# Optimization experiments

Measured on AMD Instinct MI355X. Metric: run time of the kernel, lower is better.

Reference implementation:

```python
import jax, jax.numpy as jnp
import numpy as np

D = 256; N_GRU = 4; L = 3; RATIO = 0.8; B = 64; PAD = 0
VOCAB = 50000; N = 20000; E = 320000; T = 16


def setup_inputs() -> dict:
    key = jax.random.key(0)
    ks = jax.random.split(key, 10)
    s = 0.05
    return {
        "x_tokens": jax.random.randint(ks[0], (N, T), 0, VOCAB),
        "edge_index": jax.random.randint(ks[1], (2, E), 0, N),
        "batch": jnp.sort(jax.random.randint(ks[2], (N,), 0, B)),
        "embed": jax.random.normal(ks[3], (VOCAB, D)) * s,
        "ggc_W": jax.random.normal(ks[4], (L, N_GRU, D, D)) * s,
        "gru_Wih": jax.random.normal(ks[5], (L, 3 * D, D)) * s,
        "gru_Whh": jax.random.normal(ks[6], (L, 3 * D, D)) * s,
        "gru_bih": jnp.zeros((L, 3 * D)),
        "gru_bhh": jnp.zeros((L, 3 * D)),
        "topk_p": jax.random.normal(ks[7], (L, D)) * s,
        "gate_W": jax.random.normal(ks[8], (D, 1)) * s,
        "gate_b": jnp.zeros((1,)),
    }


def gru_cell(m, h, Wih, Whh, bih, bhh):
    gi = m @ Wih.T + bih
    gh = h @ Whh.T + bhh
    i_r, i_z, i_n = jnp.split(gi, 3, axis=-1)
    h_r, h_z, h_n = jnp.split(gh, 3, axis=-1)
    r = jax.nn.sigmoid(i_r + h_r)
    z = jax.nn.sigmoid(i_z + h_z)
    n = jnp.tanh(i_n + r * h_n)
    return (1.0 - z) * n + z * h


def gated_graph_conv(h, src, dst, emask, W, Wih, Whh, bih, bhh):
    # PyG GatedGraphConv: per step, transform then scatter-add source->target, then GRU update
    for l in range(N_GRU):
        msg = (h @ W[l])[src] * emask[:, None]            # [E, D]
        agg = jax.ops.segment_sum(msg, dst, num_segments=h.shape[0])
        h = gru_cell(agg, h, Wih, Whh, bih, bhh)
    return h


def topk_pool(x, p, nmask, batch, src, dst, emask):
    # PyG TopKPooling: score = tanh(x.p/||p||), keep top ceil(ratio*n) per graph, x *= score
    score = jnp.tanh((x @ p) / jnp.linalg.norm(p))
    skey = jnp.where(nmask, score, -1e9)
    order = jnp.lexsort((-skey, batch))                   # by graph asc, score desc
    counts = jax.ops.segment_sum(jnp.ones((N,), jnp.int32), batch, num_segments=B)
    starts = jnp.cumsum(counts) - counts
    rank = jnp.zeros((N,), jnp.int32).at[order].set(
        jnp.arange(N, dtype=jnp.int32) - starts[batch[order]])
    n_valid = jax.ops.segment_sum(nmask.astype(jnp.int32), batch, num_segments=B)
    k = jnp.ceil(RATIO * n_valid.astype(jnp.float32)).astype(jnp.int32)
    keep = nmask & (rank < k[batch])
    x_new = jnp.where(keep[:, None], x * score[:, None], 0.0)
    emask_new = emask * keep[src].astype(emask.dtype) * keep[dst].astype(emask.dtype)
    return x_new, keep, emask_new


def global_att(x, nmask, batch, gW, gb):
    # GlobalAttention: segment softmax of Linear(x,1), weighted sum per graph
    logit = jnp.where(nmask, (x @ gW)[:, 0] + gb[0], -1e9)
    mx = jax.ops.segment_max(logit, batch, num_segments=B)
    e = jnp.where(nmask, jnp.exp(logit - mx[batch]), 0.0)
    denom = jax.ops.segment_sum(e, batch, num_segments=B)
    gate = e / jnp.maximum(denom[batch], 1e-12)
    return jax.ops.segment_sum(gate[:, None] * x, batch, num_segments=B)


def reference(x_tokens, edge_index, batch, embed, ggc_W, gru_Wih, gru_Whh,
              gru_bih, gru_bhh, topk_p, gate_W, gate_b):
    # STEncoder: embed token ids, mean-pool non-pad tokens per node
    tok_mask = (x_tokens != PAD)
    emb = embed[x_tokens] * tok_mask[..., None]
    h = emb.sum(1) / jnp.maximum(tok_mask.sum(1, keepdims=True), 1).astype(emb.dtype)
    src, dst = edge_index[0], edge_index[1]
    nmask = jnp.ones((N,), bool)
    emask = jnp.ones((E,), h.dtype)
    out = jnp.zeros((B, D), h.dtype)
    for l in range(L):
        h = jax.nn.relu(gated_graph_conv(h, src, dst, emask, ggc_W[l],
                                         gru_Wih[l], gru_Whh[l], gru_bih[l], gru_bhh[l]))
        h, nmask, emask = topk_pool(h, topk_p[l], nmask, batch, src, dst, emask)
        out = out + global_att(h, nmask, batch, gate_W, gate_b)
    return out
```

## Files before the change

### kernel.cpp

```cpp
#include <hip/hip_runtime.h>
#include <hip/hip_bf16.h>

namespace {

constexpr int NN = 20000;
constexpr int TT = 16;
constexpr int DD = 256;
constexpr int EE = 320000;
constexpr int BB = 64;
constexpr int NLAY = 3;
constexpr int NGRUS = 4;
constexpr int D3 = 768;
constexpr int NRB = 157;
constexpr int NXCD = 8;

typedef __bf16 bf16x8 __attribute__((ext_vector_type(8)));
typedef float  f32x4  __attribute__((ext_vector_type(4)));

__device__ __forceinline__ float us2f(unsigned short u){
  union { unsigned int i; float f; } v; v.i = ((unsigned int)u) << 16; return v.f;
}
__device__ __forceinline__ unsigned short f2us(float f){
  union { float f; unsigned int i; } v; v.f = f;
  unsigned int r = v.i + 0x7fff + ((v.i >> 16) & 1);
  return (unsigned short)(r >> 16);
}

__device__ __forceinline__ void gload16(const unsigned short* g, unsigned short* l){
  __builtin_amdgcn_global_load_lds(
      (const __attribute__((address_space(1))) unsigned int*)g,
      (__attribute__((address_space(3))) unsigned int*)l, 16, 0, 0);
}

__global__ void k_init(int* __restrict__ deg, int* __restrict__ cursor,
                       int* __restrict__ nmask, float* __restrict__ out){
  int i = blockIdx.x*256 + threadIdx.x;
  if (i < NN){ deg[i] = 0; cursor[i] = 0; nmask[i] = 1; }
  if (i < BB*DD) out[i] = 0.f;
}

__global__ void k_embed(const int* __restrict__ xt, const float* __restrict__ emb,
                        unsigned short* __restrict__ h){
  int n = blockIdx.x; int d = threadIdx.x;
  __shared__ int toks[TT];
  if (threadIdx.x < TT) toks[threadIdx.x] = xt[n*TT + threadIdx.x];
  __syncthreads();
  float acc = 0.f; int cnt = 0;
  #pragma unroll
  for (int t = 0; t < TT; ++t){
    int tk = toks[t];
    if (tk != 0){ ++cnt; acc += emb[(size_t)tk*DD + d]; }
  }
  h[(size_t)n*DD + d] = f2us(acc / (float)(cnt > 0 ? cnt : 1));
}

__global__ __launch_bounds__(256) void k_wf(const float* __restrict__ W,
                                            const float* __restrict__ Wih,
                                            unsigned short* __restrict__ WFThi,
                                            unsigned short* __restrict__ WFTlo){
  int lg = blockIdx.z; int l = lg / NGRUS;
  const float* A  = W   + (size_t)lg*DD*DD;
  const float* Bm = Wih + (size_t)l*D3*DD;
  unsigned short* oh = WFThi + (size_t)lg*D3*DD;
  unsigned short* ol = WFTlo + (size_t)lg*D3*DD;
  int k0 = blockIdx.y*64, j0 = blockIdx.x*64;
  __shared__ float sA[16][68], sB[16][68];
  int tid = threadIdx.x, ty = tid/16, tx = tid%16;
  float acc[4][4] = {};
  int m = tid >> 2, dg = (tid & 3)*4;
  for (int d0 = 0; d0 < DD; d0 += 16){
    float4 ua = *reinterpret_cast<const float4*>(A  + (size_t)(k0+m)*DD + d0+dg);
    float4 ub = *reinterpret_cast<const float4*>(Bm + (size_t)(j0+m)*DD + d0+dg);
    __syncthreads();
    sA[dg+0][m]=ua.x; sA[dg+1][m]=ua.y; sA[dg+2][m]=ua.z; sA[dg+3][m]=ua.w;
    sB[dg+0][m]=ub.x; sB[dg+1][m]=ub.y; sB[dg+2][m]=ub.z; sB[dg+3][m]=ub.w;
    __syncthreads();
    #pragma unroll
    for (int dd = 0; dd < 16; ++dd){
      float a[4], b[4];
      #pragma unroll
      for (int i=0;i<4;++i) a[i] = sA[dd][ty*4+i];
      #pragma unroll
      for (int j=0;j<4;++j) b[j] = sB[dd][tx*4+j];
      #pragma unroll
      for (int i=0;i<4;++i)
        #pragma unroll
        for (int j=0;j<4;++j) acc[i][j] += a[i]*b[j];
    }
  }
  for (int i=0;i<4;++i){
    int k = k0 + ty*4 + i;
    for (int j=0;j<4;++j){
      int c = j0 + tx*4 + j;
      float v = acc[i][j];
      unsigned short hi = f2us(v);
      float rem = v - us2f(hi);
      oh[(size_t)c*DD + k] = hi;
      ol[(size_t)c*DD + k] = f2us(rem);
    }
  }
}

__global__ void k_whh_split(const float* __restrict__ Whh, unsigned short* __restrict__ hi,
                            unsigned short* __restrict__ lo){
  size_t i = (size_t)blockIdx.x*256 + threadIdx.x;
  if (i >= (size_t)NLAY*D3*DD) return;
  float w = Whh[i];
  unsigned short h = f2us(w);
  hi[i] = h; lo[i] = f2us(w - us2f(h));
}

__global__ void k_deg(const int* __restrict__ dst, int* __restrict__ deg){
  int e = blockIdx.x*256 + threadIdx.x; if (e < EE) atomicAdd(&deg[dst[e]], 1);
}
__global__ void k_scan(const int* __restrict__ deg, int* __restrict__ offs){
  __shared__ int part[1024];
  int t = threadIdx.x; const int CH = 20;
  int base = t*CH; int s = 0;
  for (int i = 0; i < CH; ++i){ int idx = base+i; if (idx < NN) s += deg[idx]; }
  part[t] = s; __syncthreads();
  for (int o = 1; o < 1024; o <<= 1){
    int v = part[t]; int add = (t >= o) ? part[t-o] : 0;
    __syncthreads(); part[t] = v + add; __syncthreads();
  }
  int run = (t > 0) ? part[t-1] : 0;
  for (int i = 0; i < CH; ++i){ int idx = base+i; if (idx < NN){ offs[idx] = run; run += deg[idx]; } }
  if (t == 1023) offs[NN] = run;
}
__global__ void k_fill_csr(const int* __restrict__ src, const int* __restrict__ dst,
                           const int* __restrict__ offs, int* __restrict__ cursor,
                           int* __restrict__ csr_src){
  int e = blockIdx.x*256 + threadIdx.x; if (e >= EE) return;
  int d = dst[e]; int pos = atomicAdd(&cursor[d], 1);
  csr_src[offs[d] + pos] = src[e];
}

__global__ void k_bounds(const int* __restrict__ batch, int* __restrict__ starts65){
  int n = blockIdx.x*256 + threadIdx.x;
  if (n >= NN) return;
  int b = batch[n];
  int p = (n == 0) ? -1 : batch[n-1];
  for (int bb = p+1; bb <= b; ++bb) starts65[bb] = n;
  if (n == NN-1){
    for (int bb = b+1; bb <= BB; ++bb) starts65[bb] = NN;
  }
}
__global__ void k_cnts(const int* __restrict__ starts65, int* __restrict__ counts){
  int b = threadIdx.x;
  if (b < BB) counts[b] = starts65[b+1] - starts65[b];
}

__global__ void k_agg(const unsigned short* __restrict__ h, const int* __restrict__ offs,
                      const int* __restrict__ csr_src, unsigned short* __restrict__ agg){
  int wid = threadIdx.x >> 6, lane = threadIdx.x & 63;
  int n = blockIdx.x*4 + wid;
  if (n >= NN) return;
  int s = offs[n], e = offs[n+1];
  float a0 = 0.f, a1 = 0.f, a2 = 0.f, a3 = 0.f;
  int slot = s;
  for (; slot + 2 <= e; slot += 2){
    int s0 = csr_src[slot], s1 = csr_src[slot+1];
    ushort4 v0 = *reinterpret_cast<const ushort4*>(h + (size_t)s0*DD + lane*4);
    ushort4 v1 = *reinterpret_cast<const ushort4*>(h + (size_t)s1*DD + lane*4);
    a0 += us2f(v0.x) + us2f(v1.x);
    a1 += us2f(v0.y) + us2f(v1.y);
    a2 += us2f(v0.z) + us2f(v1.z);
    a3 += us2f(v0.w) + us2f(v1.w);
  }
  if (slot < e){
    int s0 = csr_src[slot];
    ushort4 v0 = *reinterpret_cast<const ushort4*>(h + (size_t)s0*DD + lane*4);
    a0 += us2f(v0.x); a1 += us2f(v0.y); a2 += us2f(v0.z); a3 += us2f(v0.w);
  }
  ushort4 o;
  o.x = f2us(a0); o.y = f2us(a1); o.z = f2us(a2); o.w = f2us(a3);
  *reinterpret_cast<ushort4*>(agg + (size_t)n*DD + lane*4) = o;
}

__global__ __launch_bounds__(256) void k_gru(
    const unsigned short* __restrict__ Ag, const unsigned short* __restrict__ Ah,
    const unsigned short* __restrict__ WfH, const unsigned short* __restrict__ WfL,
    const unsigned short* __restrict__ WhH, const unsigned short* __restrict__ WhL,
    const float* __restrict__ bih, const float* __restrict__ bhh,
    const int* __restrict__ nmask, unsigned short* __restrict__ Hn, int do_relu){
  __shared__ unsigned short sB[2][2][96*64];
  int t = threadIdx.x;
  int wv = t >> 6, lane = t & 63;
  int lr = lane & 15, kg = lane >> 4;

  int w = blockIdx.x;
  int q = (w & 7)*NRB + (w >> 3);
  int r0 = (q >> 3) * 128;
  int g0 = q & 7;

  int sw   = ((lane & 7) ^ (lane >> 3)) * 8;
  int rloc = lane >> 3;

  auto stageBoth = [&](int buf, int a){
    const unsigned short* mH = (a & 4) ? WhH : WfH;
    const unsigned short* mL = (a & 4) ? WhL : WfL;
    int kin0 = (a & 3) * 64;
    #pragma unroll
    for (int i = 0; i < 3; ++i){
      int brow = (wv + i*4)*8;
      int gate = brow >> 5;
      size_t srow = (size_t)(gate*256 + g0*32 + (brow & 31) + rloc)*DD + kin0 + sw;
      gload16(mH + srow, &sB[buf][0][brow*64]);
      gload16(mL + srow, &sB[buf][1][brow*64]);
    }
  };

  f32x4 aR[2][2], aZ[2][2], aNi[2][2], aNh[2][2];
  #pragma unroll
  for (int rf = 0; rf < 2; ++rf)
    #pragma unroll
    for (int h2 = 0; h2 < 2; ++h2){
      aR[rf][h2] = (f32x4){0.f,0.f,0.f,0.f};  aZ[rf][h2] = (f32x4){0.f,0.f,0.f,0.f};
      aNi[rf][h2] = (f32x4){0.f,0.f,0.f,0.f}; aNh[rf][h2] = (f32x4){0.f,0.f,0.f,0.f};
    }

  size_t arow0 = (size_t)(r0 + wv*32 + lr) * DD;
  size_t arow1 = (size_t)(r0 + wv*32 + 16 + lr) * DD;

  bf16x8 aF0[2][2], aF1[2][2];
  #pragma unroll
  for (int kk2 = 0; kk2 < 2; ++kk2){
    aF0[0][kk2] = *reinterpret_cast<const bf16x8*>(Ag + arow0 + kk2*32 + kg*8);
    aF1[0][kk2] = *reinterpret_cast<const bf16x8*>(Ag + arow1 + kk2*32 + kg*8);
  }
  stageBoth(0, 0);

  #pragma unroll
  for (int a = 0; a < 8; ++a){
    int buf = a & 1;
    int par = a & 1;
    __syncthreads();
    if (a < 7){
      stageBoth(buf ^ 1, a + 1);
      const unsigned short* An = ((a+1) & 4) ? Ah : Ag;
      int kinn = ((a+1) & 3) * 64;
      #pragma unroll
      for (int kk2 = 0; kk2 < 2; ++kk2){
        aF0[par ^ 1][kk2] = *reinterpret_cast<const bf16x8*>(An + arow0 + kinn + kk2*32 + kg*8);
        aF1[par ^ 1][kk2] = *reinterpret_cast<const bf16x8*>(An + arow1 + kinn + kk2*32 + kg*8);
      }
    }
    int half = (a >> 2) & 1;
    __builtin_amdgcn_s_setprio(1);
    #pragma unroll
    for (int ph = 0; ph < 2; ++ph){
      #pragma unroll
      for (int kk2 = 0; kk2 < 2; ++kk2){
        int cs = ((kk2*4 + kg) ^ (lr & 7)) * 8;
        bf16x8 a0 = aF0[par][kk2];
        bf16x8 a1 = aF1[par][kk2];
        #pragma unroll
        for (int h2 = 0; h2 < 2; ++h2){
          bf16x8 bR = *reinterpret_cast<const bf16x8*>(&sB[buf][ph][(      h2*16 + lr)*64 + cs]);
          bf16x8 bZ = *reinterpret_cast<const bf16x8*>(&sB[buf][ph][(32  + h2*16 + lr)*64 + cs]);
          bf16x8 bN = *reinterpret_cast<const bf16x8*>(&sB[buf][ph][(64  + h2*16 + lr)*64 + cs]);
          aR[0][h2] = __builtin_amdgcn_mfma_f32_16x16x32_bf16(a0, bR, aR[0][h2], 0, 0, 0);
          aR[1][h2] = __builtin_amdgcn_mfma_f32_16x16x32_bf16(a1, bR, aR[1][h2], 0, 0, 0);
          aZ[0][h2] = __builtin_amdgcn_mfma_f32_16x16x32_bf16(a0, bZ, aZ[0][h2], 0, 0, 0);
          aZ[1][h2] = __builtin_amdgcn_mfma_f32_16x16x32_bf16(a1, bZ, aZ[1][h2], 0, 0, 0);
          if (half){
            aNh[0][h2] = __builtin_amdgcn_mfma_f32_16x16x32_bf16(a0, bN, aNh[0][h2], 0, 0, 0);
            aNh[1][h2] = __builtin_amdgcn_mfma_f32_16x16x32_bf16(a1, bN, aNh[1][h2], 0, 0, 0);
          } else {
            aNi[0][h2] = __builtin_amdgcn_mfma_f32_16x16x32_bf16(a0, bN, aNi[0][h2], 0, 0, 0);
            aNi[1][h2] = __builtin_amdgcn_mfma_f32_16x16x32_bf16(a1, bN, aNi[1][h2], 0, 0, 0);
          }
        }
      }
    }
    __builtin_amdgcn_s_setprio(0);
  }

  #pragma unroll
  for (int h2 = 0; h2 < 2; ++h2){
    int col = g0*32 + h2*16 + lr;
    float bRv = bih[col]       + bhh[col];
    float bZv = bih[256 + col] + bhh[256 + col];
    float bN1 = bih[512 + col];
    float bN2 = bhh[512 + col];
    #pragma unroll
    for (int rf = 0; rf < 2; ++rf){
      #pragma unroll
      for (int j = 0; j < 4; ++j){
        int row = r0 + wv*32 + rf*16 + kg*4 + j;
        if (row < NN){
          float r = 1.f/(1.f + expf(-(aR[rf][h2][j] + bRv)));
          float z = 1.f/(1.f + expf(-(aZ[rf][h2][j] + bZv)));
          float nv = tanhf(aNi[rf][h2][j] + bN1 + r*(aNh[rf][h2][j] + bN2));
          float ho = us2f(Ah[(size_t)row*DD + col]);
          float o = (1.f - z)*nv + z*ho;
          if (do_relu) o = fmaxf(o, 0.f);
          if (!nmask[row]) o = 0.f;
          Hn[(size_t)row*DD + col] = f2us(o);
        }
      }
    }
  }
}

__global__ void k_score(const unsigned short* __restrict__ h, const float* __restrict__ p,
                        float* __restrict__ score){
  int wid = threadIdx.x >> 6, lane = threadIdx.x & 63;
  int n = blockIdx.x*4 + wid; if (n >= NN) return;
  ushort4 hu = *reinterpret_cast<const ushort4*>(h + (size_t)n*DD + lane*4);
  float4 pv = *reinterpret_cast<const float4*>(p + lane*4);
  float dot = us2f(hu.x)*pv.x + us2f(hu.y)*pv.y + us2f(hu.z)*pv.z + us2f(hu.w)*pv.w;
  float pp = pv.x*pv.x + pv.y*pv.y + pv.z*pv.z + pv.w*pv.w;
  for (int o = 32; o; o >>= 1){ dot += __shfl_down(dot, o); pp += __shfl_down(pp, o); }
  if (lane == 0) score[n] = tanhf(dot / sqrtf(pp));
}

__global__ void k_topk(const float* __restrict__ score, const int* __restrict__ starts,
                       const int* __restrict__ counts, int* __restrict__ nmask){
  int b = blockIdx.x; int st = starts[b]; int cnt = min(counts[b], 1024);
  __shared__ float sc[1024]; __shared__ int ired[256];
  int t = threadIdx.x;
  int myvalid = 0;
  for (int i = t; i < cnt; i += 256){
    int node = st + i; int v = nmask[node];
    sc[i] = v ? score[node] : -1e30f;
    myvalid += v;
  }
  ired[t] = myvalid; __syncthreads();
  for (int o = 128; o; o >>= 1){ if (t < o) ired[t] += ired[t+o]; __syncthreads(); }
  int nv = ired[0];
  int k = (4*nv + 4)/5;
  __syncthreads();
  for (int i = t; i < cnt; i += 256){
    float si = sc[i]; int node = st + i; int keep = 0;
    if (si > -1e29f){
      int rank = 0;
      for (int j = 0; j < cnt; ++j){
        float sj = sc[j];
        rank += (sj > si) || (sj == si && j < i);
      }
      keep = (rank < k);
    }
    nmask[node] = keep;
  }
}

__global__ void k_scale(unsigned short* __restrict__ h, const float* __restrict__ score,
                        const int* __restrict__ nmask){
  int idx = blockIdx.x*256 + threadIdx.x;
  int n = idx >> 8;
  unsigned short v = nmask[n] ? f2us(us2f(h[idx])*score[n]) : (unsigned short)0;
  h[idx] = v;
}

__global__ void k_att(const unsigned short* __restrict__ h, const float* __restrict__ gW,
                      const float* __restrict__ gb, const int* __restrict__ starts,
                      const int* __restrict__ counts, const int* __restrict__ nmask,
                      float* __restrict__ outacc){
  int b = blockIdx.x; int st = starts[b]; int cnt = min(counts[b], 1024);
  __shared__ float lg[1024]; __shared__ float red[256];
  int t = threadIdx.x, wid = t >> 6, lane = t & 63;
  float gbv = gb[0];
  for (int i = wid; i < cnt; i += 4){
    int node = st + i;
    ushort4 hu = *reinterpret_cast<const ushort4*>(h + (size_t)node*DD + lane*4);
    float4 wv = *reinterpret_cast<const float4*>(gW + lane*4);
    float dot = us2f(hu.x)*wv.x + us2f(hu.y)*wv.y + us2f(hu.z)*wv.z + us2f(hu.w)*wv.w;
    for (int o = 32; o; o >>= 1) dot += __shfl_down(dot, o);
    if (lane == 0) lg[i] = nmask[node] ? dot + gbv : -1e30f;
  }
  __syncthreads();
  float mx = -1e30f;
  for (int i = t; i < cnt; i += 256) mx = fmaxf(mx, lg[i]);
  red[t] = mx; __syncthreads();
  for (int o = 128; o; o >>= 1){ if (t < o) red[t] = fmaxf(red[t], red[t+o]); __syncthreads(); }
  mx = red[0]; __syncthreads();
  float se = 0.f;
  for (int i = t; i < cnt; i += 256){
    float e = (lg[i] > -1e29f) ? expf(lg[i] - mx) : 0.f;
    lg[i] = e; se += e;
  }
  red[t] = se; __syncthreads();
  for (int o = 128; o; o >>= 1){ if (t < o) red[t] += red[t+o]; __syncthreads(); }
  float denom = fmaxf(red[0], 1e-12f);
  __syncthreads();
  float a0=0.f,a1=0.f,a2=0.f,a3=0.f;
  int i = 0;
  for (; i + 4 <= cnt; i += 4){
    a0 += lg[i+0]*us2f(h[(size_t)(st+i+0)*DD + t]);
    a1 += lg[i+1]*us2f(h[(size_t)(st+i+1)*DD + t]);
    a2 += lg[i+2]*us2f(h[(size_t)(st+i+2)*DD + t]);
    a3 += lg[i+3]*us2f(h[(size_t)(st+i+3)*DD + t]);
  }
  for (; i < cnt; ++i) a0 += lg[i]*us2f(h[(size_t)(st+i)*DD + t]);
  outacc[(size_t)b*DD + t] += (a0+a1+a2+a3)/denom;
}

}

extern "C" void kernel_launch(void* const* d_in, const int* in_sizes, int n_in,
                              void* d_out, int out_size, void* d_ws, size_t ws_size,
                              hipStream_t stream){
  const int*   x_tokens = (const int*)d_in[0];
  const int*   e_src    = (const int*)d_in[1];
  const int*   e_dst    = e_src + EE;
  const int*   batch    = (const int*)d_in[2];
  const float* embed    = (const float*)d_in[3];
  const float* ggcW     = (const float*)d_in[4];
  const float* gWih     = (const float*)d_in[5];
  const float* gWhh     = (const float*)d_in[6];
  const float* gbih     = (const float*)d_in[7];
  const float* gbhh     = (const float*)d_in[8];
  const float* topkp    = (const float*)d_in[9];
  const float* gateW    = (const float*)d_in[10];
  const float* gateb    = (const float*)d_in[11];
  (void)in_sizes; (void)n_in; (void)out_size;
  float* out = (float*)d_out;

  char* ws = (char*)d_ws;
  size_t off = 0;
  auto carve = [&](size_t bytes)->char*{
    char* p = ws + off;
    off += (bytes + 255) & ~(size_t)255;
    return p;
  };
  unsigned short* h0    = (unsigned short*)carve((size_t)NN*DD*2);
  unsigned short* h1    = (unsigned short*)carve((size_t)NN*DD*2);
  unsigned short* agg   = (unsigned short*)carve((size_t)NN*DD*2);
  unsigned short* WFThi = (unsigned short*)carve((size_t)NLAY*NGRUS*D3*DD*2);
  unsigned short* WFTlo = (unsigned short*)carve((size_t)NLAY*NGRUS*D3*DD*2);
  unsigned short* WhhHi = (unsigned short*)carve((size_t)NLAY*D3*DD*2);
  unsigned short* WhhLo = (unsigned short*)carve((size_t)NLAY*D3*DD*2);
  float* score   = (float*)carve((size_t)NN*4);
  int* nmask     = (int*)carve((size_t)NN*4);
  int* deg       = (int*)carve((size_t)NN*4);
  int* cursor    = (int*)carve((size_t)NN*4);
  int* offs      = (int*)carve((size_t)(NN+1)*4);
  int* csr_src   = (int*)carve((size_t)EE*4);
  int* counts    = (int*)carve((size_t)BB*4);
  int* starts    = (int*)carve((size_t)(BB+1)*4);
  if (off > ws_size) return;

  k_init<<<(NN+255)/256, 256, 0, stream>>>(deg, cursor, nmask, out);
  k_embed<<<NN, DD, 0, stream>>>(x_tokens, embed, h0);
  k_wf<<<dim3(D3/64, DD/64, NLAY*NGRUS), 256, 0, stream>>>(ggcW, gWih, WFThi, WFTlo);
  k_whh_split<<<(NLAY*D3*DD + 255)/256, 256, 0, stream>>>(gWhh, WhhHi, WhhLo);
  k_deg<<<(EE+255)/256, 256, 0, stream>>>(e_dst, deg);
  k_scan<<<1, 1024, 0, stream>>>(deg, offs);
  k_fill_csr<<<(EE+255)/256, 256, 0, stream>>>(e_src, e_dst, offs, cursor, csr_src);
  k_bounds<<<(NN+255)/256, 256, 0, stream>>>(batch, starts);
  k_cnts<<<1, 64, 0, stream>>>(starts, counts);

  unsigned short* hc = h0; unsigned short* hn = h1;
  for (int l = 0; l < NLAY; ++l){
    const unsigned short* WhHl = WhhHi + (size_t)l*D3*DD;
    const unsigned short* WhLl = WhhLo + (size_t)l*D3*DD;
    const float* bihl = gbih + (size_t)l*D3;
    const float* bhhl = gbhh + (size_t)l*D3;
    for (int g = 0; g < NGRUS; ++g){
      const unsigned short* WfHl = WFThi + (size_t)(l*NGRUS+g)*D3*DD;
      const unsigned short* WfLl = WFTlo + (size_t)(l*NGRUS+g)*D3*DD;
      k_agg<<<(NN+3)/4, 256, 0, stream>>>(hc, offs, csr_src, agg);
      k_gru<<<NRB*NXCD, 256, 0, stream>>>(agg, hc, WfHl, WfLl, WhHl, WhLl,
                                          bihl, bhhl, nmask, hn,
                                          (g == NGRUS-1) ? 1 : 0);
      unsigned short* tmp = hc; hc = hn; hn = tmp;
    }
    k_score<<<NN/4, 256, 0, stream>>>(hc, topkp + (size_t)l*DD, score);
    k_topk<<<BB, 256, 0, stream>>>(score, starts, counts, nmask);
    k_scale<<<NN, 256, 0, stream>>>(hc, score, nmask);
    k_att<<<BB, 256, 0, stream>>>(hc, gateW, gateb, starts, counts, nmask, out);
  }
}
```

Measured before the change: 1.374 ms.

## Double GRU row tile to 256 and batch CSR index loads in aggregation

The fused GRU GEMM kernel now gives each block 256 rows instead of 128. Each wave handles four 16-row fragments, so every staged weight tile in LDS is reused across twice as many rows, and the grid shrinks accordingly. The neighbour aggregation kernel now loads up to 64 CSR source indices per wave in one coalesced load, broadcasts them with shuffles, and unrolls the gather four deep. The larger tile raises accumulator and A-fragment register use, which may lower occupancy. A small padding buffer is added to the workspace to absorb the out-of-range row reads from the last tile.

```diff
diff --git a/kernel.cpp b/kernel.cpp
--- a/kernel.cpp
+++ b/kernel.cpp
@@ -11,7 +11,7 @@
 constexpr int NLAY = 3;
 constexpr int NGRUS = 4;
 constexpr int D3 = 768;
-constexpr int NRB = 157;
+constexpr int NRB2 = 79;
 constexpr int NXCD = 8;
 
 typedef __bf16 bf16x8 __attribute__((ext_vector_type(8)));
@@ -157,20 +157,27 @@
   if (n >= NN) return;
   int s = offs[n], e = offs[n+1];
   float a0 = 0.f, a1 = 0.f, a2 = 0.f, a3 = 0.f;
-  int slot = s;
-  for (; slot + 2 <= e; slot += 2){
-    int s0 = csr_src[slot], s1 = csr_src[slot+1];
-    ushort4 v0 = *reinterpret_cast<const ushort4*>(h + (size_t)s0*DD + lane*4);
-    ushort4 v1 = *reinterpret_cast<const ushort4*>(h + (size_t)s1*DD + lane*4);
-    a0 += us2f(v0.x) + us2f(v1.x);
-    a1 += us2f(v0.y) + us2f(v1.y);
-    a2 += us2f(v0.z) + us2f(v1.z);
-    a3 += us2f(v0.w) + us2f(v1.w);
-  }
-  if (slot < e){
-    int s0 = csr_src[slot];
-    ushort4 v0 = *reinterpret_cast<const ushort4*>(h + (size_t)s0*DD + lane*4);
-    a0 += us2f(v0.x); a1 += us2f(v0.y); a2 += us2f(v0.z); a3 += us2f(v0.w);
+  for (int base = s; base < e; base += 64){
+    int cnt = min(64, e - base);
+    int idx = (lane < cnt) ? csr_src[base + lane] : 0;
+    int i = 0;
+    for (; i + 4 <= cnt; i += 4){
+      int s0 = __shfl(idx, i+0), s1 = __shfl(idx, i+1);
+      int s2 = __shfl(idx, i+2), s3 = __shfl(idx, i+3);
+      ushort4 v0 = *reinterpret_cast<const ushort4*>(h + (size_t)s0*DD + lane*4);
+      ushort4 v1 = *reinterpret_cast<const ushort4*>(h + (size_t)s1*DD + lane*4);
+      ushort4 v2 = *reinterpret_cast<const ushort4*>(h + (size_t)s2*DD + lane*4);
+      ushort4 v3 = *reinterpret_cast<const ushort4*>(h + (size_t)s3*DD + lane*4);
+      a0 += us2f(v0.x); a1 += us2f(v0.y); a2 += us2f(v0.z); a3 += us2f(v0.w);
+      a0 += us2f(v1.x); a1 += us2f(v1.y); a2 += us2f(v1.z); a3 += us2f(v1.w);
+      a0 += us2f(v2.x); a1 += us2f(v2.y); a2 += us2f(v2.z); a3 += us2f(v2.w);
+      a0 += us2f(v3.x); a1 += us2f(v3.y); a2 += us2f(v3.z); a3 += us2f(v3.w);
+    }
+    for (; i < cnt; ++i){
+      int s0 = __shfl(idx, i);
+      ushort4 v0 = *reinterpret_cast<const ushort4*>(h + (size_t)s0*DD + lane*4);
+      a0 += us2f(v0.x); a1 += us2f(v0.y); a2 += us2f(v0.z); a3 += us2f(v0.w);
+    }
   }
   ushort4 o;
   o.x = f2us(a0); o.y = f2us(a1); o.z = f2us(a2); o.w = f2us(a3);
@@ -189,8 +196,8 @@
   int lr = lane & 15, kg = lane >> 4;
 
   int w = blockIdx.x;
-  int q = (w & 7)*NRB + (w >> 3);
-  int r0 = (q >> 3) * 128;
+  int q = (w & 7)*NRB2 + (w >> 3);
+  int r0 = (q >> 3) * 256;
   int g0 = q & 7;
 
   int sw   = ((lane & 7) ^ (lane >> 3)) * 8;
@@ -210,24 +217,26 @@
     }
   };
 
-  f32x4 aR[2][2], aZ[2][2], aNi[2][2], aNh[2][2];
-  #pragma unroll
-  for (int rf = 0; rf < 2; ++rf)
+  f32x4 aR[4][2], aZ[4][2], aNi[4][2], aNh[4][2];
+  #pragma unroll
+  for (int rf = 0; rf < 4; ++rf)
     #pragma unroll
     for (int h2 = 0; h2 < 2; ++h2){
       aR[rf][h2] = (f32x4){0.f,0.f,0.f,0.f};  aZ[rf][h2] = (f32x4){0.f,0.f,0.f,0.f};
       aNi[rf][h2] = (f32x4){0.f,0.f,0.f,0.f}; aNh[rf][h2] = (f32x4){0.f,0.f,0.f,0.f};
     }
 
-  size_t arow0 = (size_t)(r0 + wv*32 + lr) * DD;
-  size_t arow1 = (size_t)(r0 + wv*32 + 16 + lr) * DD;
-
-  bf16x8 aF0[2][2], aF1[2][2];
-  #pragma unroll
-  for (int kk2 = 0; kk2 < 2; ++kk2){
-    aF0[0][kk2] = *reinterpret_cast<const bf16x8*>(Ag + arow0 + kk2*32 + kg*8);
-    aF1[0][kk2] = *reinterpret_cast<const bf16x8*>(Ag + arow1 + kk2*32 + kg*8);
-  }
+  size_t arow[4];
+  #pragma unroll
+  for (int rf = 0; rf < 4; ++rf)
+    arow[rf] = (size_t)(r0 + wv*64 + rf*16 + lr) * DD;
+
+  bf16x8 aF[2][4][2];
+  #pragma unroll
+  for (int rf = 0; rf < 4; ++rf)
+    #pragma unroll
+    for (int kk2 = 0; kk2 < 2; ++kk2)
+      aF[0][rf][kk2] = *reinterpret_cast<const bf16x8*>(Ag + arow[rf] + kk2*32 + kg*8);
   stageBoth(0, 0);
 
   #pragma unroll
@@ -240,10 +249,11 @@
       const unsigned short* An = ((a+1) & 4) ? Ah : Ag;
       int kinn = ((a+1) & 3) * 64;
       #pragma unroll
-      for (int kk2 = 0; kk2 < 2; ++kk2){
-        aF0[par ^ 1][kk2] = *reinterpret_cast<const bf16x8*>(An + arow0 + kinn + kk2*32 + kg*8);
-        aF1[par ^ 1][kk2] = *reinterpret_cast<const bf16x8*>(An + arow1 + kinn + kk2*32 + kg*8);
-      }
+      for (int rf = 0; rf < 4; ++rf)
+        #pragma unroll
+        for (int kk2 = 0; kk2 < 2; ++kk2)
+          aF[par ^ 1][rf][kk2] =
+              *reinterpret_cast<const bf16x8*>(An + arow[rf] + kinn + kk2*32 + kg*8);
     }
     int half = (a >> 2) & 1;
     __builtin_amdgcn_s_setprio(1);
@@ -252,23 +262,20 @@
       #pragma unroll
       for (int kk2 = 0; kk2 < 2; ++kk2){
         int cs = ((kk2*4 + kg) ^ (lr & 7)) * 8;
-        bf16x8 a0 = aF0[par][kk2];
-        bf16x8 a1 = aF1[par][kk2];
         #pragma unroll
         for (int h2 = 0; h2 < 2; ++h2){
           bf16x8 bR = *reinterpret_cast<const bf16x8*>(&sB[buf][ph][(      h2*16 + lr)*64 + cs]);
           bf16x8 bZ = *reinterpret_cast<const bf16x8*>(&sB[buf][ph][(32  + h2*16 + lr)*64 + cs]);
           bf16x8 bN = *reinterpret_cast<const bf16x8*>(&sB[buf][ph][(64  + h2*16 + lr)*64 + cs]);
-          aR[0][h2] = __builtin_amdgcn_mfma_f32_16x16x32_bf16(a0, bR, aR[0][h2], 0, 0, 0);
-          aR[1][h2] = __builtin_amdgcn_mfma_f32_16x16x32_bf16(a1, bR, aR[1][h2], 0, 0, 0);
-          aZ[0][h2] = __builtin_amdgcn_mfma_f32_16x16x32_bf16(a0, bZ, aZ[0][h2], 0, 0, 0);
-          aZ[1][h2] = __builtin_amdgcn_mfma_f32_16x16x32_bf16(a1, bZ, aZ[1][h2], 0, 0, 0);
-          if (half){
-            aNh[0][h2] = __builtin_amdgcn_mfma_f32_16x16x32_bf16(a0, bN, aNh[0][h2], 0, 0, 0);
-            aNh[1][h2] = __builtin_amdgcn_mfma_f32_16x16x32_bf16(a1, bN, aNh[1][h2], 0, 0, 0);
-          } else {
-            aNi[0][h2] = __builtin_amdgcn_mfma_f32_16x16x32_bf16(a0, bN, aNi[0][h2], 0, 0, 0);
-            aNi[1][h2] = __builtin_amdgcn_mfma_f32_16x16x32_bf16(a1, bN, aNi[1][h2], 0, 0, 0);
+          #pragma unroll
+          for (int rf = 0; rf < 4; ++rf){
+            bf16x8 av = aF[par][rf][kk2];
+            aR[rf][h2] = __builtin_amdgcn_mfma_f32_16x16x32_bf16(av, bR, aR[rf][h2], 0, 0, 0);
+            aZ[rf][h2] = __builtin_amdgcn_mfma_f32_16x16x32_bf16(av, bZ, aZ[rf][h2], 0, 0, 0);
+            if (half)
+              aNh[rf][h2] = __builtin_amdgcn_mfma_f32_16x16x32_bf16(av, bN, aNh[rf][h2], 0, 0, 0);
+            else
+              aNi[rf][h2] = __builtin_amdgcn_mfma_f32_16x16x32_bf16(av, bN, aNi[rf][h2], 0, 0, 0);
           }
         }
       }
@@ -284,10 +291,10 @@
     float bN1 = bih[512 + col];
     float bN2 = bhh[512 + col];
     #pragma unroll
-    for (int rf = 0; rf < 2; ++rf){
+    for (int rf = 0; rf < 4; ++rf){
       #pragma unroll
       for (int j = 0; j < 4; ++j){
-        int row = r0 + wv*32 + rf*16 + kg*4 + j;
+        int row = r0 + wv*64 + rf*16 + kg*4 + j;
         if (row < NN){
           float r = 1.f/(1.f + expf(-(aR[rf][h2][j] + bRv)));
           float z = 1.f/(1.f + expf(-(aZ[rf][h2][j] + bZv)));
@@ -439,6 +446,7 @@
   int* csr_src   = (int*)carve((size_t)EE*4);
   int* counts    = (int*)carve((size_t)BB*4);
   int* starts    = (int*)carve((size_t)(BB+1)*4);
+  carve((size_t)256*DD*2);
   if (off > ws_size) return;
 
   k_init<<<(NN+255)/256, 256, 0, stream>>>(deg, cursor, nmask, out);
@@ -461,9 +469,9 @@
       const unsigned short* WfHl = WFThi + (size_t)(l*NGRUS+g)*D3*DD;
       const unsigned short* WfLl = WFTlo + (size_t)(l*NGRUS+g)*D3*DD;
       k_agg<<<(NN+3)/4, 256, 0, stream>>>(hc, offs, csr_src, agg);
-      k_gru<<<NRB*NXCD, 256, 0, stream>>>(agg, hc, WfHl, WfLl, WhHl, WhLl,
-                                          bihl, bhhl, nmask, hn,
-                                          (g == NGRUS-1) ? 1 : 0);
+      k_gru<<<NRB2*NXCD, 256, 0, stream>>>(agg, hc, WfHl, WfLl, WhHl, WhLl,
+                                           bihl, bhhl, nmask, hn,
+                                           (g == NGRUS-1) ? 1 : 0);
       unsigned short* tmp = hc; hc = hn; hn = tmp;
     }
     k_score<<<NN/4, 256, 0, stream>>>(hc, topkp + (size_t)l*DD, score);
```

After: 1.549 ms. +12.7%, slower.
